# Optimization experiments

Measured on AMD Instinct MI355X. Metric: run time of the kernel, lower is better.

The kernel has to match this reference:

```python
import jax, jax.numpy as jnp
import numpy as np

N, L, S, D, H = 4, 8192, 8192, 256, 8
DH = D // H  # 32
EPS_ATTN = 1e-6
EPS_LN = 1e-5


def setup_inputs() -> dict:
    key = jax.random.key(0)
    ks = jax.random.split(key, 8)
    w = lambda k, sh: jax.random.normal(k, sh, jnp.float32) * 0.02
    return {
        "x": jax.random.normal(ks[0], (N, L, D), jnp.float32),
        "source": jax.random.normal(ks[1], (N, S, D), jnp.float32),
        "Wq": w(ks[2], (D, D)),
        "Wk": w(ks[3], (D, D)),
        "Wv": w(ks[4], (D, D)),
        "Wm": w(ks[5], (D, D)),
        "W1": w(ks[6], (2 * D, 2 * D)),
        "W2": w(ks[7], (2 * D, D)),
        "g1": jnp.ones((D,), jnp.float32),
        "b1": jnp.zeros((D,), jnp.float32),
        "g2": jnp.ones((D,), jnp.float32),
        "b2": jnp.zeros((D,), jnp.float32),
    }


def _layernorm(x, g, b):
    m = jnp.mean(x, axis=-1, keepdims=True)
    v = jnp.var(x, axis=-1, keepdims=True)
    return (x - m) * jax.lax.rsqrt(v + EPS_LN) * g + b


def reference(x, source, Wq, Wk, Wv, Wm, W1, W2, g1, b1, g2, b2):
    bs = x.shape[0]
    # QKV projections (bias=False), split heads -> [N, L/S, H, DH]
    q = (x @ Wq).reshape(bs, -1, H, DH)
    k = (source @ Wk).reshape(bs, -1, H, DH)
    v = (source @ Wv).reshape(bs, -1, H, DH)
    # elu+1 feature map (linear attention, LoFTR-style)
    Q = jax.nn.elu(q) + 1.0
    K = jax.nn.elu(k) + 1.0
    v_len = v.shape[1]
    vals = v / v_len
    KV = jnp.einsum("nshd,nshv->nhdv", K, vals)  # [N, H, DH, DH]
    Z = 1.0 / (jnp.einsum("nlhd,nhd->nlh", Q, K.sum(axis=1)) + EPS_ATTN)
    msg = jnp.einsum("nlhd,nhdv,nlh->nlhv", Q, KV, Z) * v_len  # [N, L, H, DH]
    # merge heads + LN
    msg = msg.reshape(bs, -1, H * DH) @ Wm
    msg = _layernorm(msg, g1, b1)
    # concat-MLP with LeakyReLU(0.1)
    h = jnp.concatenate([x, msg], axis=2) @ W1
    h = jnp.where(h >= 0, h, 0.1 * h)
    msg = h @ W2
    msg = _layernorm(msg, g2, b2)
    return x + msg
```

## Files before the change

kernel.cpp:

```cpp
#include <hip/hip_runtime.h>

typedef __bf16 bf16;
typedef __bf16 bf16x4 __attribute__((ext_vector_type(4)));
typedef __bf16 bf16x8 __attribute__((ext_vector_type(8)));
typedef float f32x4 __attribute__((ext_vector_type(4)));

#define BM 128
#define BN 128
#define BK 64

__device__ __forceinline__ float apply_epi(float v, int epi) {
  if (epi == 1) return v > 0.f ? v + 1.f : __expf(v);
  if (epi == 2) return v >= 0.f ? v : 0.1f * v;
  return v;
}

__device__ __forceinline__ void g2l16(const bf16* gp, bf16* lp) {
  __builtin_amdgcn_global_load_lds(
      (const __attribute__((address_space(1))) void*)gp,
      (__attribute__((address_space(3))) void*)lp, 16, 0, 0);
}

__global__ void detect_kernel(const unsigned* g1raw, int* flag) {
  if (threadIdx.x == 0 && blockIdx.x == 0)
    *flag = (g1raw[0] == 0x3F800000u) ? 1 : 0;
}

struct TransArgs {
  const void* src[6];
  bf16* dst[6];
  int R[6], C[6], t0[6];
};

__global__ __launch_bounds__(256) void prep_kernel(
    const void* __restrict__ xin, const void* __restrict__ sin,
    bf16* __restrict__ bx, bf16* __restrict__ bs,
    TransArgs ta, const int* flagp) {
  const bool f32 = (*flagp != 0);
  if (blockIdx.x < 8192) {
    const void* s;
    bf16* d;
    size_t i;
    if (blockIdx.x < 4096) {
      s = xin; d = bx; i = (size_t)blockIdx.x * 2048 + threadIdx.x * 8;
    } else {
      s = sin; d = bs; i = (size_t)(blockIdx.x - 4096) * 2048 + threadIdx.x * 8;
    }
    if (f32) {
      f32x4 lo = *(const f32x4*)((const float*)s + i);
      f32x4 hi = *(const f32x4*)((const float*)s + i + 4);
      bf16x8 t;
      t[0] = (bf16)lo[0]; t[1] = (bf16)lo[1]; t[2] = (bf16)lo[2]; t[3] = (bf16)lo[3];
      t[4] = (bf16)hi[0]; t[5] = (bf16)hi[1]; t[6] = (bf16)hi[2]; t[7] = (bf16)hi[3];
      *(bf16x8*)(d + i) = t;
    } else {
      *(bf16x8*)(d + i) = *(const bf16x8*)((const bf16*)s + i);
    }
    return;
  }
  __shared__ bf16 tile[32][33];
  int bid = blockIdx.x - 8192;
  int si = 0;
#pragma unroll
  for (int i = 1; i < 6; ++i)
    if (bid >= ta.t0[i]) si = i;
  const void* srcv = ta.src[si];
  bf16* dst = ta.dst[si];
  int R = ta.R[si], Cc = ta.C[si];
  int lt = bid - ta.t0[si];
  int tpr = Cc >> 5;
  int tr = lt / tpr, tc = lt % tpr;
  int tx = threadIdx.x & 31, ty0 = threadIdx.x >> 5;
#pragma unroll
  for (int i = 0; i < 4; ++i) {
    int ty = ty0 + i * 8;
    size_t idx = (size_t)(tr * 32 + ty) * Cc + tc * 32 + tx;
    tile[ty][tx] = f32 ? (bf16)((const float*)srcv)[idx] : ((const bf16*)srcv)[idx];
  }
  __syncthreads();
#pragma unroll
  for (int i = 0; i < 4; ++i) {
    int ty = ty0 + i * 8;
    dst[(size_t)(tc * 32 + ty) * R + tr * 32 + tx] = tile[tx][ty];
  }
}

__global__ __launch_bounds__(256) void gemm_rt(
    const bf16* __restrict__ A, const bf16* __restrict__ A2, int ldA,
    const bf16* __restrict__ Bt, bf16* __restrict__ C, int Nn, int Kk, int epi) {
  __shared__ bf16 As[BM * BK];
  __shared__ bf16 Bs[BN * BK];
  const int tid = threadIdx.x;
  const int m0 = blockIdx.x * BM;
  const int n0 = blockIdx.y * BN;
  const int wave = tid >> 6, lane = tid & 63;
  const int wm = (wave & 1) * 64, wn = (wave >> 1) * 64;
  const int q = lane >> 4, mr = lane & 15;

  f32x4 acc[4][4];
#pragma unroll
  for (int i = 0; i < 4; ++i)
#pragma unroll
    for (int j = 0; j < 4; ++j) acc[i][j] = (f32x4){0.f, 0.f, 0.f, 0.f};

  const int kTiles = Kk / BK;
  for (int kt = 0; kt < kTiles; ++kt) {
    int kk = kt * BK;
    const bf16* Ab = A;
    int kcol = kk;
    if (A2 && kk >= 256) { Ab = A2; kcol = kk - 256; }
    __syncthreads();
#pragma unroll
    for (int it = 0; it < 4; ++it) {
      int id = it * 256 + tid;
      int rr = id >> 3, pp = id & 7;
      g2l16(Ab + (size_t)(m0 + rr) * ldA + kcol + pp * 8, &As[id * 8]);
    }
#pragma unroll
    for (int it = 0; it < 4; ++it) {
      int id = it * 256 + tid;
      int rr = id >> 3, pp = id & 7;
      g2l16(Bt + (size_t)(n0 + rr) * Kk + kk + pp * 8, &Bs[id * 8]);
    }
    __syncthreads();
#pragma unroll
    for (int ks = 0; ks < 2; ++ks) {
      bf16x8 af[4], bfv[4];
#pragma unroll
      for (int mi = 0; mi < 4; ++mi)
        af[mi] = *(const bf16x8*)&As[(wm + mi * 16 + mr) * BK + (ks * 4 + q) * 8];
#pragma unroll
      for (int ni = 0; ni < 4; ++ni)
        bfv[ni] = *(const bf16x8*)&Bs[(wn + ni * 16 + mr) * BK + (ks * 4 + q) * 8];
#pragma unroll
      for (int mi = 0; mi < 4; ++mi)
#pragma unroll
        for (int ni = 0; ni < 4; ++ni)
          acc[mi][ni] = __builtin_amdgcn_mfma_f32_16x16x32_bf16(af[mi], bfv[ni], acc[mi][ni], 0, 0, 0);
    }
  }

#pragma unroll
  for (int mi = 0; mi < 4; ++mi)
#pragma unroll
    for (int ni = 0; ni < 4; ++ni)
#pragma unroll
      for (int r4 = 0; r4 < 4; ++r4) {
        int row = m0 + wm + mi * 16 + q * 4 + r4;
        int cn = n0 + wn + ni * 16 + mr;
        float v = apply_epi(acc[mi][ni][r4], epi);
        C[(size_t)row * Nn + cn] = (bf16)v;
      }
}

#define KVCH 256
__global__ __launch_bounds__(256) void kv_kernel(
    const bf16* __restrict__ Kf, const bf16* __restrict__ V,
    float* __restrict__ partial, float* __restrict__ pk) {
  __shared__ bf16 Ks[KVCH][32];
  __shared__ bf16 Vs[KVCH][32];
  const int cb = blockIdx.x, h = blockIdx.y, n = blockIdx.z;
  const int tid = threadIdx.x;
  const int wave = tid >> 6, lane = tid & 63;
  const int d0 = (lane & 7) * 4, dv0 = (lane >> 3) * 4;
  const int s0 = cb * KVCH;
#pragma unroll
  for (int rd = 0; rd < 4; ++rd) {
    int rr = rd * 64 + (tid >> 2), pp = tid & 3;
    size_t g = ((size_t)(n * 8192 + s0 + rr)) * 256 + h * 32 + pp * 8;
    *(bf16x8*)&Ks[rr][pp * 8] = *(const bf16x8*)(Kf + g);
    *(bf16x8*)&Vs[rr][pp * 8] = *(const bf16x8*)(V + g);
  }
  __syncthreads();
  float acc[4][4] = {};
  float ks4[4] = {};
#pragma unroll 4
  for (int si = 0; si < 64; ++si) {
    int s = wave * 64 + si;
    bf16x4 k4 = *(const bf16x4*)&Ks[s][d0];
    bf16x4 v4 = *(const bf16x4*)&Vs[s][dv0];
    float kf[4] = {(float)k4[0], (float)k4[1], (float)k4[2], (float)k4[3]};
    float vf[4] = {(float)v4[0], (float)v4[1], (float)v4[2], (float)v4[3]};
#pragma unroll
    for (int vi = 0; vi < 4; ++vi)
#pragma unroll
      for (int di = 0; di < 4; ++di) acc[vi][di] = fmaf(vf[vi], kf[di], acc[vi][di]);
#pragma unroll
    for (int di = 0; di < 4; ++di) ks4[di] += kf[di];
  }
  __syncthreads();
  float* red = (float*)&Ks[0][0];
  float* ksr = (float*)&Vs[0][0];
#pragma unroll
  for (int vi = 0; vi < 4; ++vi)
#pragma unroll
    for (int di = 0; di < 4; ++di)
      red[wave * 1024 + (dv0 + vi) * 32 + d0 + di] = acc[vi][di];
  if (dv0 == 0) {
#pragma unroll
    for (int di = 0; di < 4; ++di) ksr[wave * 32 + d0 + di] = ks4[di];
  }
  __syncthreads();
  const size_t slot = (size_t)(n * 8 + h) * 32 + cb;
  f32x4 s4 = {0.f, 0.f, 0.f, 0.f};
#pragma unroll
  for (int w = 0; w < 4; ++w) s4 += *(const f32x4*)&red[w * 1024 + tid * 4];
  *(f32x4*)&partial[slot * 1024 + tid * 4] = s4;
  if (tid < 32) {
    float ss = 0.f;
#pragma unroll
    for (int w = 0; w < 4; ++w) ss += ksr[w * 32 + tid];
    pk[slot * 32 + tid] = ss;
  }
}

__global__ __launch_bounds__(256) void kv_reduce(
    const float* __restrict__ partial, const float* __restrict__ pk,
    float* __restrict__ kv_acc, float* __restrict__ ksum) {
  const int b = blockIdx.x;
  const int t = threadIdx.x;
  f32x4 s4 = {0.f, 0.f, 0.f, 0.f};
  for (int c = 0; c < 32; ++c)
    s4 += *(const f32x4*)&partial[((size_t)b * 32 + c) * 1024 + t * 4];
  *(f32x4*)&kv_acc[(size_t)b * 1024 + t * 4] = s4;
  if (t < 32) {
    float ss = 0.f;
    for (int c = 0; c < 32; ++c) ss += pk[((size_t)b * 32 + c) * 32 + t];
    ksum[(size_t)b * 32 + t] = ss;
  }
}

__global__ __launch_bounds__(256) void msg_kernel(
    const bf16* __restrict__ Q, const float* __restrict__ kv_acc,
    const float* __restrict__ ksum, bf16* __restrict__ msg) {
  __shared__ bf16 kvt[8][32][32];
  __shared__ float ksl[8][32];
  __shared__ float zl[8][128];
  int tid = threadIdx.x;
  int row0 = blockIdx.x * 128;
  int n = row0 >> 13;
  const float* kvb = kv_acc + (size_t)n * 8192;
  for (int i = tid; i < 8192; i += 256) ((bf16*)kvt)[i] = (bf16)kvb[i];
  ((float*)ksl)[tid] = ksum[(size_t)n * 256 + tid];
  __syncthreads();
  int r = tid & 127, hg = tid >> 7;
  const bf16* qrow = Q + (size_t)(row0 + r) * 256;
#pragma unroll
  for (int hh = 0; hh < 4; ++hh) {
    int h = hg * 4 + hh;
    float dot = 0.f;
#pragma unroll
    for (int d = 0; d < 32; ++d) dot = fmaf((float)qrow[h * 32 + d], ksl[h][d], dot);
    zl[h][r] = 1.f / (dot + 1e-6f);
  }
  __syncthreads();
  int wave = tid >> 6, lane = tid & 63, q = lane >> 4, mr = lane & 15;
  f32x4 zero = {0.f, 0.f, 0.f, 0.f};
  for (int h = 0; h < 8; ++h) {
    bf16x8 b0 = *(const bf16x8*)&kvt[h][mr][q * 8];
    bf16x8 b1 = *(const bf16x8*)&kvt[h][16 + mr][q * 8];
#pragma unroll
    for (int mi = 0; mi < 2; ++mi) {
      int arow = wave * 32 + mi * 16 + mr;
      bf16x8 a = *(const bf16x8*)(Q + (size_t)(row0 + arow) * 256 + h * 32 + q * 8);
      f32x4 c0 = __builtin_amdgcn_mfma_f32_16x16x32_bf16(a, b0, zero, 0, 0, 0);
      f32x4 c1 = __builtin_amdgcn_mfma_f32_16x16x32_bf16(a, b1, zero, 0, 0, 0);
#pragma unroll
      for (int r4 = 0; r4 < 4; ++r4) {
        int orow = wave * 32 + mi * 16 + q * 4 + r4;
        float z = zl[h][orow];
        size_t ob = (size_t)(row0 + orow) * 256 + h * 32;
        msg[ob + mr] = (bf16)(c0[r4] * z);
        msg[ob + 16 + mr] = (bf16)(c1[r4] * z);
      }
    }
  }
}

__global__ __launch_bounds__(256) void ln_kernel(
    const bf16* __restrict__ in, const void* __restrict__ g, const void* __restrict__ b,
    const void* __restrict__ resid, void* __restrict__ outp,
    const int* flagp, int ioDual) {
  const bool gbF32 = (*flagp != 0);
  const bool ioF32 = ioDual && gbF32;
  int wave = threadIdx.x >> 6, lane = threadIdx.x & 63;
  size_t row = (size_t)blockIdx.x * 4 + wave;
  int c = lane * 4;
  bf16x4 v = *(const bf16x4*)(in + row * 256 + c);
  float x0 = (float)v[0], x1 = (float)v[1], x2 = (float)v[2], x3 = (float)v[3];
  float s = x0 + x1 + x2 + x3;
  float sq = x0 * x0 + x1 * x1 + x2 * x2 + x3 * x3;
#pragma unroll
  for (int o = 32; o > 0; o >>= 1) {
    s += __shfl_xor(s, o);
    sq += __shfl_xor(sq, o);
  }
  float mean = s * (1.f / 256.f);
  float var = sq * (1.f / 256.f) - mean * mean;
  float rstd = rsqrtf(var + 1e-5f);
  float g0, g1v, g2v, g3, b0, b1v, b2v, b3;
  if (gbF32) {
    f32x4 gv = *(const f32x4*)((const float*)g + c);
    f32x4 bv = *(const f32x4*)((const float*)b + c);
    g0 = gv[0]; g1v = gv[1]; g2v = gv[2]; g3 = gv[3];
    b0 = bv[0]; b1v = bv[1]; b2v = bv[2]; b3 = bv[3];
  } else {
    bf16x4 gv = *(const bf16x4*)((const bf16*)g + c);
    bf16x4 bv = *(const bf16x4*)((const bf16*)b + c);
    g0 = (float)gv[0]; g1v = (float)gv[1]; g2v = (float)gv[2]; g3 = (float)gv[3];
    b0 = (float)bv[0]; b1v = (float)bv[1]; b2v = (float)bv[2]; b3 = (float)bv[3];
  }
  float y0 = (x0 - mean) * rstd * g0 + b0;
  float y1 = (x1 - mean) * rstd * g1v + b1v;
  float y2 = (x2 - mean) * rstd * g2v + b2v;
  float y3 = (x3 - mean) * rstd * g3 + b3;
  if (resid) {
    if (ioF32) {
      f32x4 rv = *(const f32x4*)((const float*)resid + row * 256 + c);
      y0 += rv[0]; y1 += rv[1]; y2 += rv[2]; y3 += rv[3];
    } else {
      bf16x4 rv = *(const bf16x4*)((const bf16*)resid + row * 256 + c);
      y0 += (float)rv[0]; y1 += (float)rv[1]; y2 += (float)rv[2]; y3 += (float)rv[3];
    }
  }
  if (ioF32) {
    f32x4 o4 = {y0, y1, y2, y3};
    *(f32x4*)((float*)outp + row * 256 + c) = o4;
  } else {
    bf16x4 o4;
    o4[0] = (bf16)y0; o4[1] = (bf16)y1; o4[2] = (bf16)y2; o4[3] = (bf16)y3;
    *(bf16x4*)((bf16*)outp + row * 256 + c) = o4;
  }
}

extern "C" void kernel_launch(void* const* d_in, const int* in_sizes, int n_in,
                              void* d_out, int out_size, void* d_ws, size_t ws_size,
                              hipStream_t stream) {
  const void* x   = d_in[0];
  const void* src = d_in[1];
  const void* Wq  = d_in[2];
  const void* Wk  = d_in[3];
  const void* Wv  = d_in[4];
  const void* Wm  = d_in[5];
  const void* W1  = d_in[6];
  const void* W2  = d_in[7];
  const void* g1  = d_in[8];
  const void* b1  = d_in[9];
  const void* g2  = d_in[10];
  const void* b2  = d_in[11];

  char* ws = (char*)d_ws;
  bf16* bufA = (bf16*)(ws);
  bf16* bufB = (bf16*)(ws + ((size_t)16 << 20));
  bf16* bufC = (bf16*)(ws + ((size_t)32 << 20));
  bf16* WqT = (bf16*)(ws + ((size_t)48 << 20));
  bf16* WkT = WqT + 65536;
  bf16* WvT = WkT + 65536;
  bf16* WmT = WvT + 65536;
  bf16* W1T = WmT + 65536;
  bf16* W2T = W1T + 262144;
  float* kv_acc = (float*)(ws + ((size_t)50 << 20));
  float* ksum = kv_acc + 32768;
  int* flagp = (int*)(ws + ((size_t)50 << 20) + 160 * 1024);
  float* partial = (float*)(ws + ((size_t)51 << 20));
  float* pk = (float*)(ws + ((size_t)55 << 20));
  bf16* bufX = (bf16*)d_out;
  bf16* bufS = bufX + 8388608;

  detect_kernel<<<dim3(1), dim3(64), 0, stream>>>((const unsigned*)g1, flagp);

  TransArgs ta;
  ta.src[0] = Wq; ta.src[1] = Wk; ta.src[2] = Wv; ta.src[3] = Wm; ta.src[4] = W1; ta.src[5] = W2;
  ta.dst[0] = WqT; ta.dst[1] = WkT; ta.dst[2] = WvT; ta.dst[3] = WmT; ta.dst[4] = W1T; ta.dst[5] = W2T;
  ta.R[0] = 256; ta.R[1] = 256; ta.R[2] = 256; ta.R[3] = 256; ta.R[4] = 512; ta.R[5] = 512;
  ta.C[0] = 256; ta.C[1] = 256; ta.C[2] = 256; ta.C[3] = 256; ta.C[4] = 512; ta.C[5] = 256;
  ta.t0[0] = 0; ta.t0[1] = 64; ta.t0[2] = 128; ta.t0[3] = 192; ta.t0[4] = 256; ta.t0[5] = 512;
  prep_kernel<<<dim3(8832), dim3(256), 0, stream>>>(x, src, bufX, bufS, ta, flagp);

  gemm_rt<<<dim3(256, 2), dim3(256), 0, stream>>>(bufX, nullptr, 256, WqT, bufA, 256, 256, 1);
  gemm_rt<<<dim3(256, 2), dim3(256), 0, stream>>>(bufS, nullptr, 256, WkT, bufB, 256, 256, 1);
  gemm_rt<<<dim3(256, 2), dim3(256), 0, stream>>>(bufS, nullptr, 256, WvT, bufC, 256, 256, 0);

  kv_kernel<<<dim3(32, 8, 4), dim3(256), 0, stream>>>(bufB, bufC, partial, pk);
  kv_reduce<<<dim3(32), dim3(256), 0, stream>>>(partial, pk, kv_acc, ksum);

  msg_kernel<<<dim3(256), dim3(256), 0, stream>>>(bufA, kv_acc, ksum, bufB);

  gemm_rt<<<dim3(256, 2), dim3(256), 0, stream>>>(bufB, nullptr, 256, WmT, bufA, 256, 256, 0);

  ln_kernel<<<dim3(8192), dim3(256), 0, stream>>>(bufA, g1, b1, nullptr, bufC, flagp, 0);

  gemm_rt<<<dim3(256, 4), dim3(256), 0, stream>>>(bufX, bufC, 256, W1T, bufA, 512, 512, 2);

  gemm_rt<<<dim3(256, 2), dim3(256), 0, stream>>>(bufA, nullptr, 512, W2T, bufC, 256, 512, 0);

  ln_kernel<<<dim3(8192), dim3(256), 0, stream>>>(bufC, g2, b2, x, d_out, flagp, 1);
}
```

Before: 298.2 us.

## Fuse K and V projections into one GEMM and XOR-swizzle LDS tiles

The K and V projection GEMMs now run as one launch over a concatenated transposed weight, and the output columns are routed to two buffers with separate epilogues. This removes a launch and a second read of the source activations. The LDS tile layout is also XOR-swizzled by row so the fragment reads for MFMA avoid bank conflicts. The shared read of the source tensor now depends on L2 reuse across column blocks.

```diff
diff --git a/kernel.cpp b/kernel.cpp
--- a/kernel.cpp
+++ b/kernel.cpp
@@ -87,7 +87,8 @@
 
 __global__ __launch_bounds__(256) void gemm_rt(
     const bf16* __restrict__ A, const bf16* __restrict__ A2, int ldA,
-    const bf16* __restrict__ Bt, bf16* __restrict__ C, int Nn, int Kk, int epi) {
+    const bf16* __restrict__ Bt, bf16* __restrict__ C, int Nn, int Kk, int epi,
+    bf16* __restrict__ C2, int epi2, int split) {
   __shared__ bf16 As[BM * BK];
   __shared__ bf16 Bs[BN * BK];
   const int tid = threadIdx.x;
@@ -113,25 +114,29 @@
 #pragma unroll
     for (int it = 0; it < 4; ++it) {
       int id = it * 256 + tid;
-      int rr = id >> 3, pp = id & 7;
-      g2l16(Ab + (size_t)(m0 + rr) * ldA + kcol + pp * 8, &As[id * 8]);
+      int rr = id >> 3, pp = id & 7, gg = pp ^ (rr & 7);
+      g2l16(Ab + (size_t)(m0 + rr) * ldA + kcol + gg * 8, &As[id * 8]);
     }
 #pragma unroll
     for (int it = 0; it < 4; ++it) {
       int id = it * 256 + tid;
-      int rr = id >> 3, pp = id & 7;
-      g2l16(Bt + (size_t)(n0 + rr) * Kk + kk + pp * 8, &Bs[id * 8]);
+      int rr = id >> 3, pp = id & 7, gg = pp ^ (rr & 7);
+      g2l16(Bt + (size_t)(n0 + rr) * Kk + kk + gg * 8, &Bs[id * 8]);
     }
     __syncthreads();
 #pragma unroll
     for (int ks = 0; ks < 2; ++ks) {
       bf16x8 af[4], bfv[4];
 #pragma unroll
-      for (int mi = 0; mi < 4; ++mi)
-        af[mi] = *(const bf16x8*)&As[(wm + mi * 16 + mr) * BK + (ks * 4 + q) * 8];
-#pragma unroll
-      for (int ni = 0; ni < 4; ++ni)
-        bfv[ni] = *(const bf16x8*)&Bs[(wn + ni * 16 + mr) * BK + (ks * 4 + q) * 8];
+      for (int mi = 0; mi < 4; ++mi) {
+        int rrow = wm + mi * 16 + mr;
+        af[mi] = *(const bf16x8*)&As[rrow * BK + ((ks * 4 + q) ^ (rrow & 7)) * 8];
+      }
+#pragma unroll
+      for (int ni = 0; ni < 4; ++ni) {
+        int rrow = wn + ni * 16 + mr;
+        bfv[ni] = *(const bf16x8*)&Bs[rrow * BK + ((ks * 4 + q) ^ (rrow & 7)) * 8];
+      }
 #pragma unroll
       for (int mi = 0; mi < 4; ++mi)
 #pragma unroll
@@ -140,6 +145,9 @@
     }
   }
 
+  bf16* Cw = C;
+  int nbase = n0, ep = epi;
+  if (C2 && n0 >= split) { Cw = C2; nbase = n0 - split; ep = epi2; }
 #pragma unroll
   for (int mi = 0; mi < 4; ++mi)
 #pragma unroll
@@ -147,9 +155,9 @@
 #pragma unroll
       for (int r4 = 0; r4 < 4; ++r4) {
         int row = m0 + wm + mi * 16 + q * 4 + r4;
-        int cn = n0 + wn + ni * 16 + mr;
-        float v = apply_epi(acc[mi][ni][r4], epi);
-        C[(size_t)row * Nn + cn] = (bf16)v;
+        int cn = nbase + wn + ni * 16 + mr;
+        float v = apply_epi(acc[mi][ni][r4], ep);
+        Cw[(size_t)row * Nn + cn] = (bf16)v;
       }
 }
 
@@ -353,12 +361,11 @@
   bf16* bufA = (bf16*)(ws);
   bf16* bufB = (bf16*)(ws + ((size_t)16 << 20));
   bf16* bufC = (bf16*)(ws + ((size_t)32 << 20));
-  bf16* WqT = (bf16*)(ws + ((size_t)48 << 20));
-  bf16* WkT = WqT + 65536;
-  bf16* WvT = WkT + 65536;
-  bf16* WmT = WvT + 65536;
-  bf16* W1T = WmT + 65536;
-  bf16* W2T = W1T + 262144;
+  bf16* WqT  = (bf16*)(ws + ((size_t)48 << 20));
+  bf16* WkvT = WqT + 65536;
+  bf16* WmT  = WkvT + 131072;
+  bf16* W1T  = WmT + 65536;
+  bf16* W2T  = W1T + 262144;
   float* kv_acc = (float*)(ws + ((size_t)50 << 20));
   float* ksum = kv_acc + 32768;
   int* flagp = (int*)(ws + ((size_t)50 << 20) + 160 * 1024);
@@ -371,28 +378,32 @@
 
   TransArgs ta;
   ta.src[0] = Wq; ta.src[1] = Wk; ta.src[2] = Wv; ta.src[3] = Wm; ta.src[4] = W1; ta.src[5] = W2;
-  ta.dst[0] = WqT; ta.dst[1] = WkT; ta.dst[2] = WvT; ta.dst[3] = WmT; ta.dst[4] = W1T; ta.dst[5] = W2T;
+  ta.dst[0] = WqT; ta.dst[1] = WkvT; ta.dst[2] = WkvT + 65536; ta.dst[3] = WmT; ta.dst[4] = W1T; ta.dst[5] = W2T;
   ta.R[0] = 256; ta.R[1] = 256; ta.R[2] = 256; ta.R[3] = 256; ta.R[4] = 512; ta.R[5] = 512;
   ta.C[0] = 256; ta.C[1] = 256; ta.C[2] = 256; ta.C[3] = 256; ta.C[4] = 512; ta.C[5] = 256;
   ta.t0[0] = 0; ta.t0[1] = 64; ta.t0[2] = 128; ta.t0[3] = 192; ta.t0[4] = 256; ta.t0[5] = 512;
   prep_kernel<<<dim3(8832), dim3(256), 0, stream>>>(x, src, bufX, bufS, ta, flagp);
 
-  gemm_rt<<<dim3(256, 2), dim3(256), 0, stream>>>(bufX, nullptr, 256, WqT, bufA, 256, 256, 1);
-  gemm_rt<<<dim3(256, 2), dim3(256), 0, stream>>>(bufS, nullptr, 256, WkT, bufB, 256, 256, 1);
-  gemm_rt<<<dim3(256, 2), dim3(256), 0, stream>>>(bufS, nullptr, 256, WvT, bufC, 256, 256, 0);
+  gemm_rt<<<dim3(256, 2), dim3(256), 0, stream>>>(bufX, nullptr, 256, WqT, bufA, 256, 256, 1,
+                                                  nullptr, 0, 0);
+  gemm_rt<<<dim3(256, 4), dim3(256), 0, stream>>>(bufS, nullptr, 256, WkvT, bufB, 256, 256, 1,
+                                                  bufC, 0, 256);
 
   kv_kernel<<<dim3(32, 8, 4), dim3(256), 0, stream>>>(bufB, bufC, partial, pk);
   kv_reduce<<<dim3(32), dim3(256), 0, stream>>>(partial, pk, kv_acc, ksum);
 
   msg_kernel<<<dim3(256), dim3(256), 0, stream>>>(bufA, kv_acc, ksum, bufB);
 
-  gemm_rt<<<dim3(256, 2), dim3(256), 0, stream>>>(bufB, nullptr, 256, WmT, bufA, 256, 256, 0);
+  gemm_rt<<<dim3(256, 2), dim3(256), 0, stream>>>(bufB, nullptr, 256, WmT, bufA, 256, 256, 0,
+                                                  nullptr, 0, 0);
 
   ln_kernel<<<dim3(8192), dim3(256), 0, stream>>>(bufA, g1, b1, nullptr, bufC, flagp, 0);
 
-  gemm_rt<<<dim3(256, 4), dim3(256), 0, stream>>>(bufX, bufC, 256, W1T, bufA, 512, 512, 2);
-
-  gemm_rt<<<dim3(256, 2), dim3(256), 0, stream>>>(bufA, nullptr, 512, W2T, bufC, 256, 512, 0);
+  gemm_rt<<<dim3(256, 4), dim3(256), 0, stream>>>(bufX, bufC, 256, W1T, bufA, 512, 512, 2,
+                                                  nullptr, 0, 0);
+
+  gemm_rt<<<dim3(256, 2), dim3(256), 0, stream>>>(bufA, nullptr, 512, W2T, bufC, 256, 512, 0,
+                                                  nullptr, 0, 0);
 
   ln_kernel<<<dim3(8192), dim3(256), 0, stream>>>(bufC, g2, b2, x, d_out, flagp, 1);
 }
```

After: 286.4 us. 1.04x faster.
